# Performance work log

Hardware: AMD Instinct MI355X
Metric: run time of the kernel (lower is better)

The kernel has to match this reference:

```python
import jax, jax.numpy as jnp
import numpy as np
from jax import lax

M1_THRESHOLD = 0.03
M2_THRESHOLD = 0.3
SAMP_THRESHOLD = 0.1


def _make_filt(diag: int = 0) -> np.ndarray:
    # diag=0 -> d1 = d2 = 0: 7-point cross (6 face neighbors + center)
    d1 = 1.0 / np.sqrt(2.0) if diag else 0.0
    d2 = 1.0 / np.sqrt(3.0) if diag else 0.0
    f = np.array([[[d2, d1, d2], [d1, 1, d1], [d2, d1, d2]],
                  [[d1, 1, d1], [1, 1, 1], [d1, 1, d1]],
                  [[d2, d1, d2], [d1, 1, d1], [d2, d1, d2]]], dtype=np.float32)
    return f[None, None]  # [O=1, I=1, 3, 3, 3]


def setup_inputs() -> dict:
    key = jax.random.key(0)
    # NCDHW logit volume: 8 frames, 48 z-planes, 256x256 px
    logits = jax.random.normal(key, (8, 1, 48, 256, 256), dtype=jnp.float32)
    filt = jnp.asarray(_make_filt(diag=0))
    return {"logits": logits, "filt": filt}


def reference(logits, filt):
    p = jax.nn.sigmoid(logits)
    # clip below m1, then 3x3x3 max-pool (stride 1, pad 1)
    p_clip = jnp.where(p > M1_THRESHOLD, p, jnp.zeros_like(p))
    pool = lax.reduce_window(
        p_clip, -jnp.inf, lax.max,
        window_dimensions=(1, 1, 3, 3, 3),
        window_strides=(1, 1, 1, 1, 1),
        padding=((0, 0), (0, 0), (1, 1), (1, 1), (1, 1)))
    max_mask1 = (p == pool).astype(p.dtype)
    # 3x3x3 spatial-integration conv, pad 1
    conv = lax.conv_general_dilated(
        p, filt,
        window_strides=(1, 1, 1),
        padding=((1, 1), (1, 1), (1, 1)),
        dimension_numbers=("NCDHW", "OIDHW", "NCDHW"))
    p_ps1 = max_mask1 * conv
    p_copy = p * (1.0 - max_mask1)
    max_mask2 = (p_copy > M2_THRESHOLD).astype(p.dtype)
    p_ps = p_ps1 + max_mask2 * conv  # Probs_si
    samples = (p_ps > SAMP_THRESHOLD).astype(p.dtype)  # Samples_si
    return (p_ps, samples)
```

## Files before the change

kernel.cpp:

```cpp
#include <hip/hip_runtime.h>
#include <cmath>
#include <type_traits>

namespace {

constexpr int W = 256, H = 256, D = 48, NB = 8;
constexpr int YT = 8;
constexpr int ZC = 12;
constexpr int SR = YT + 2;
constexpr int W2 = 264;
constexpr int NPLANES = ZC + 2;

__device__ __forceinline__ float sigmoid_ref(float x) {
    float p = __fdividef(1.0f, 1.0f + __expf(-x));
    if (fabsf(p - 0.3f) < 4e-6f) {
        double pd = 1.0 / (1.0 + exp(-(double)x));
        p = (pd > 0.3) ? 0.30000025f : 0.29999995f;
    }
    return p;
}

__global__ __launch_bounds__(256, 4) void si_post_kernel(
        const float* __restrict__ logits, float* __restrict__ out) {
    const int x = threadIdx.x;
    const int id = blockIdx.x;
    const int n  = id & 7;
    const int z0 = ((id >> 3) & 3) * ZC;
    const int y0 = (id >> 5) * YT;

    __shared__ float ptile[2][SR][W2];

    const float* __restrict__ src  = logits + (size_t)n * (D * H * W);
    float* __restrict__ outp = out + (size_t)n * (D * H * W);
    float* __restrict__ outs = outp + (size_t)NB * (D * H * W);

    if (x < 2 * SR * 4) {
        const int b  = x / (SR * 4);
        const int rr = (x >> 2) % SR;
        ptile[b][rr][256 + (x & 3)] = 0.0f;
    }

    const int q0 = x, q1 = x + 256, q2 = x + 512;
    const bool has2 = (x < 128);

    auto stage_issue = [&](int i, float4& v0, float4& v1, float4& v2) {
        const int zs  = z0 - 1 + i;
        const int zcl = zs < 0 ? 0 : (zs >= D ? D - 1 : zs);
        const float4* s4 = reinterpret_cast<const float4*>(src + (size_t)zcl * (H * W));
        auto addr = [&](int q) {
            const int r = q >> 6, c4 = q & 63;
            const int y = y0 - 1 + r;
            const int ycl = y < 0 ? 0 : (y >= H ? H - 1 : y);
            return ycl * (W / 4) + c4;
        };
        v0 = s4[addr(q0)];
        v1 = s4[addr(q1)];
        if (has2) v2 = s4[addr(q2)];
    };

    auto stage_write = [&](int i, int nb, const float4& v0, const float4& v1,
                           const float4& v2) {
        const int zs  = z0 - 1 + i;
        const bool zok = (zs >= 0) && (zs < D);
        auto wr = [&](int q, const float4& v) {
            const int r = q >> 6, c4 = q & 63;
            const int y = y0 - 1 + r;
            float4 pv;
            if (zok && (unsigned)y < (unsigned)H) {
                pv.x = sigmoid_ref(v.x); pv.y = sigmoid_ref(v.y);
                pv.z = sigmoid_ref(v.z); pv.w = sigmoid_ref(v.w);
            } else {
                pv = make_float4(0.f, 0.f, 0.f, 0.f);
            }
            *reinterpret_cast<float4*>(&ptile[nb][r][c4 * 4]) = pv;
        };
        wr(q0, v0);
        wr(q1, v1);
        if (has2) wr(q2, v2);
    };

    float pmaxP[2][YT], convP[2][YT], pcH[2][YT];
    #pragma unroll
    for (int j = 0; j < YT; ++j) {
        pmaxP[0][j] = pmaxP[1][j] = 0.0f;
        convP[0][j] = convP[1][j] = 0.0f;
        pcH[0][j]   = pcH[1][j]   = 0.0f;
    }

    const int xl = (x == 0) ? 258 : (x - 1);
    const int xr = x + 1;

    auto consume = [&](auto Qc, int i, int b) {
        constexpr int Q = decltype(Qc)::value;
        const bool emit = (i >= 2);
        const int zo = z0 + i - 2;
        const float* tp = &ptile[b][0][0];
        float rmA = 0.f, rmB = 0.f, rsB = 0.f, pcA = 0.f, pcB = 0.f;
        #pragma unroll
        for (int r = 0; r < SR; ++r) {
            const float pl = tp[r * W2 + xl];
            const float pm = tp[r * W2 + x];
            const float pr = tp[r * W2 + xr];
            const float rm = fmaxf(fmaxf(pl, pm), pr);
            const float rs = (pl + pm) + pr;
            if (r >= 2) {
                const int ym = r - 2;
                const float m2d = fmaxf(fmaxf(rmA, rmB), rm);
                const float cr  = (rsB + pcA) + pm;
                const float pcc = pcB;
                if (emit) {
                    const float m    = fmaxf(pmaxP[Q][ym], m2d);
                    const float conv = convP[Q][ym] + pcc;
                    const float pcen = pcH[1 - Q][ym];
                    const float pool = (m > 0.03f) ? m : 0.0f;
                    const bool  cond = (pcen == pool) || (pcen > 0.3f);
                    const float pps  = cond ? conv : 0.0f;
                    const float smp  = (pps > 0.1f) ? 1.0f : 0.0f;
                    const int o = (zo * H + (y0 + ym)) * W + x;
                    __builtin_nontemporal_store(pps, &outp[o]);
                    __builtin_nontemporal_store(smp, &outs[o]);
                }
                pmaxP[1 - Q][ym] = fmaxf(pmaxP[1 - Q][ym], m2d);
                convP[1 - Q][ym] += cr;
                pmaxP[Q][ym] = m2d;
                convP[Q][ym] = pcc;
                pcH[Q][ym]   = pcc;
            }
            rmA = rmB; rmB = rm; rsB = rs; pcA = pcB; pcB = pm;
        }
    };

    float4 v0 = make_float4(0, 0, 0, 0), v1 = v0, v2 = v0;
    stage_issue(0, v0, v1, v2);
    stage_write(0, 0, v0, v1, v2);
    __syncthreads();

    int b = 0;
    #pragma unroll 1
    for (int i = 0; i < NPLANES; i += 2) {
        {
            const bool st = (i + 1 < NPLANES);
            if (st) stage_issue(i + 1, v0, v1, v2);
            consume(std::integral_constant<int, 0>{}, i, b);
            if (st) stage_write(i + 1, b ^ 1, v0, v1, v2);
            __syncthreads();
            b ^= 1;
        }
        {
            const bool st = (i + 2 < NPLANES);
            if (st) stage_issue(i + 2, v0, v1, v2);
            consume(std::integral_constant<int, 1>{}, i + 1, b);
            if (st) stage_write(i + 2, b ^ 1, v0, v1, v2);
            __syncthreads();
            b ^= 1;
        }
    }
}

}

extern "C" void kernel_launch(void* const* d_in, const int* in_sizes, int n_in,
                              void* d_out, int out_size, void* d_ws, size_t ws_size,
                              hipStream_t stream) {
    const float* logits = (const float*)d_in[0];
    float* out = (float*)d_out;
    si_post_kernel<<<dim3(NB * (D / ZC) * (H / YT), 1, 1), dim3(256, 1, 1), 0,
                     stream>>>(logits, out);
}
```

Baseline: 57.49 us.

## Double y-tile height per block with two 256-thread row groups sharing staged planes

Each block now covers 16 rows instead of 8, using 512 threads split into two groups that each process an 8-row sub-band from a shared 18-row staged tile. This cuts the halo overhead: 18 rows are loaded and sigmoided per 16 output rows instead of 10 per 8, so there is less redundant global reading and transcendental work. The trade-off is half as many blocks in the grid, larger shared memory per block and larger blocks, which may lower occupancy or weaken latency hiding.

New measurement: 54.17 us (median of 2 runs). 1.06x faster.

```diff
diff --git a/kernel.cpp b/kernel.cpp
--- a/kernel.cpp
+++ b/kernel.cpp
@@ -5,11 +5,13 @@
 namespace {
 
 constexpr int W = 256, H = 256, D = 48, NB = 8;
-constexpr int YT = 8;
-constexpr int ZC = 12;
-constexpr int SR = YT + 2;
-constexpr int W2 = 264;
+constexpr int YT  = 16;
+constexpr int YTS = 8;
+constexpr int ZC  = 12;
+constexpr int SR  = YT + 2;
+constexpr int W2  = 264;
 constexpr int NPLANES = ZC + 2;
+constexpr int NT = 512;
 
 __device__ __forceinline__ float sigmoid_ref(float x) {
     float p = __fdividef(1.0f, 1.0f + __expf(-x));
@@ -20,9 +22,11 @@
     return p;
 }
 
-__global__ __launch_bounds__(256, 4) void si_post_kernel(
+__global__ __launch_bounds__(NT, 4) void si_post_kernel(
         const float* __restrict__ logits, float* __restrict__ out) {
-    const int x = threadIdx.x;
+    const int tid = threadIdx.x;
+    const int x = tid & 255;
+    const int g = tid >> 8;
     const int id = blockIdx.x;
     const int n  = id & 7;
     const int z0 = ((id >> 3) & 3) * ZC;
@@ -34,14 +38,14 @@
     float* __restrict__ outp = out + (size_t)n * (D * H * W);
     float* __restrict__ outs = outp + (size_t)NB * (D * H * W);
 
-    if (x < 2 * SR * 4) {
-        const int b  = x / (SR * 4);
-        const int rr = (x >> 2) % SR;
-        ptile[b][rr][256 + (x & 3)] = 0.0f;
+    if (tid < 2 * SR * 4) {
+        const int b  = tid / (SR * 4);
+        const int rr = (tid >> 2) % SR;
+        ptile[b][rr][256 + (tid & 3)] = 0.0f;
     }
 
-    const int q0 = x, q1 = x + 256, q2 = x + 512;
-    const bool has2 = (x < 128);
+    const int q0 = tid, q1 = tid + 512, q2 = tid + 1024;
+    const bool has2 = (tid < 128);
 
     auto stage_issue = [&](int i, float4& v0, float4& v1, float4& v2) {
         const int zs  = z0 - 1 + i;
@@ -79,9 +83,9 @@
         if (has2) wr(q2, v2);
     };
 
-    float pmaxP[2][YT], convP[2][YT], pcH[2][YT];
+    float pmaxP[2][YTS], convP[2][YTS], pcH[2][YTS];
     #pragma unroll
-    for (int j = 0; j < YT; ++j) {
+    for (int j = 0; j < YTS; ++j) {
         pmaxP[0][j] = pmaxP[1][j] = 0.0f;
         convP[0][j] = convP[1][j] = 0.0f;
         pcH[0][j]   = pcH[1][j]   = 0.0f;
@@ -89,15 +93,16 @@
 
     const int xl = (x == 0) ? 258 : (x - 1);
     const int xr = x + 1;
+    const int rbase = g * YTS;
 
     auto consume = [&](auto Qc, int i, int b) {
         constexpr int Q = decltype(Qc)::value;
         const bool emit = (i >= 2);
         const int zo = z0 + i - 2;
-        const float* tp = &ptile[b][0][0];
+        const float* tp = &ptile[b][rbase][0];
         float rmA = 0.f, rmB = 0.f, rsB = 0.f, pcA = 0.f, pcB = 0.f;
         #pragma unroll
-        for (int r = 0; r < SR; ++r) {
+        for (int r = 0; r < YTS + 2; ++r) {
             const float pl = tp[r * W2 + xl];
             const float pm = tp[r * W2 + x];
             const float pr = tp[r * W2 + xr];
@@ -116,7 +121,7 @@
                     const bool  cond = (pcen == pool) || (pcen > 0.3f);
                     const float pps  = cond ? conv : 0.0f;
                     const float smp  = (pps > 0.1f) ? 1.0f : 0.0f;
-                    const int o = (zo * H + (y0 + ym)) * W + x;
+                    const int o = (zo * H + (y0 + rbase + ym)) * W + x;
                     __builtin_nontemporal_store(pps, &outp[o]);
                     __builtin_nontemporal_store(smp, &outs[o]);
                 }
@@ -164,6 +169,6 @@
                               hipStream_t stream) {
     const float* logits = (const float*)d_in[0];
     float* out = (float*)d_out;
-    si_post_kernel<<<dim3(NB * (D / ZC) * (H / YT), 1, 1), dim3(256, 1, 1), 0,
+    si_post_kernel<<<dim3(NB * (D / ZC) * (H / YT), 1, 1), dim3(NT, 1, 1), 0,
                      stream>>>(logits, out);
 }
```
